# Kernel tuning notes

Hardware: AMD Instinct MI355X
Metric: run time of the kernel (lower is better)

## Reference

```python
import jax, jax.numpy as jnp
import numpy as np

E = 21   # numParticipants (experts)
D = 128  # input features (hardcoded Linear(128,16))
H = 16   # hidden
N = 262144  # rows


def setup_inputs() -> dict:
    key = jax.random.key(0)
    ks = jax.random.split(key, 6)
    x = jax.random.normal(ks[0], (N, D), dtype=jnp.float32)
    sid = jax.random.randint(ks[1], (N,), 0, E)
    s1 = 1.0 / np.sqrt(D)
    W1 = jax.random.uniform(ks[2], (E, D, H), jnp.float32, -s1, s1)
    b1 = jax.random.uniform(ks[3], (E, H), jnp.float32, -s1, s1)
    s2 = 1.0 / np.sqrt(H)
    W2 = jax.random.uniform(ks[4], (E, H), jnp.float32, -s2, s2)  # Linear(16,1) weight, squeezed
    b2 = jax.random.uniform(ks[5], (E,), jnp.float32, -s2, s2)
    return {"x": x, "sid": sid, "W1": W1, "b1": b1, "W2": W2, "b2": b2}


def reference(x, sid, W1, b1, W2, b2):
    # Per-row expert MLP: h = relu(x @ W1[sid] + b1[sid]); y = relu(h . W2[sid] + b2[sid]).
    # Dropout(0.5) is identity in eval mode. Vectorized routing: compute first layer for
    # all 21 tiny experts ([N,E,H] ~ 350MB), then select the routed expert per row.
    h_all = jax.nn.relu(jnp.einsum('nd,edh->neh', x, W1) + b1[None, :, :])  # [N,E,H]
    h = jnp.take_along_axis(h_all, sid[:, None, None], axis=1)[:, 0, :]      # [N,H]
    y = jax.nn.relu(jnp.einsum('nh,nh->n', h, W2[sid]) + b2[sid])            # [N]
    return y[:, None]  # [N,1]
```

## Files before the change

kernel.cpp:

```cpp
#include <hip/hip_runtime.h>
#include <stdint.h>

#define N_ROWS 262144
#define DIM    128
#define HID    16
#define NEXP   21
#define NSEG   (N_ROWS / 64 + NEXP)
#define NBLK1  256
#define RPB    (N_ROWS / NBLK1)
#define RPT    (RPB / 256)

__global__ __launch_bounds__(256) void k_hist(const int* __restrict__ sid,
                                              int* __restrict__ counts,
                                              int* __restrict__ blockBase) {
    __shared__ int lh[NEXP];
    int t = threadIdx.x;
    if (t < NEXP) lh[t] = 0;
    __syncthreads();
    int base = blockIdx.x * RPB + t;
#pragma unroll
    for (int r = 0; r < RPT; r++) {
        atomicAdd(&lh[sid[base + r * 256]], 1);
    }
    __syncthreads();
    if (t < NEXP) blockBase[blockIdx.x * NEXP + t] = atomicAdd(&counts[t], lh[t]);
}

__global__ __launch_bounds__(256) void k_scatter(const int* __restrict__ sid,
                                                 const int* __restrict__ counts,
                                                 const int* __restrict__ blockBase,
                                                 int* __restrict__ buckets) {
    __shared__ int sbase[NEXP];
    __shared__ int lcur[NEXP];
    int t = threadIdx.x;
    if (t == 0) {
        int acc = 0;
        for (int e = 0; e < NEXP; e++) {
            sbase[e] = acc + blockBase[blockIdx.x * NEXP + e];
            acc += ((counts[e] + 63) >> 6) << 6;
        }
    }
    if (t < NEXP) lcur[t] = 0;
    __syncthreads();
    int base = blockIdx.x * RPB + t;
#pragma unroll
    for (int r = 0; r < RPT; r++) {
        int row = base + r * 256;
        int e = sid[row];
        int lp = atomicAdd(&lcur[e], 1);
        buckets[sbase[e] + lp] = row | (e << 24);
    }
}

typedef __attribute__((ext_vector_type(8))) short bf16x8;
typedef __attribute__((ext_vector_type(4))) float f32x4;

__device__ __forceinline__ uint32_t pack2(uint32_t a, uint32_t b) {
    return __builtin_amdgcn_perm(b, a, 0x07060302u);
}

__device__ __forceinline__ void cvt8(const float* f, bf16x8& fh, bf16x8& fl) {
    union { uint32_t u[4]; bf16x8 v; } H, L;
#pragma unroll
    for (int i = 0; i < 4; i++) {
        uint32_t a = __float_as_uint(f[2 * i]);
        uint32_t b = __float_as_uint(f[2 * i + 1]);
        H.u[i] = pack2(a, b);
        float ra = f[2 * i]     - __uint_as_float(a & 0xffff0000u);
        float rb = f[2 * i + 1] - __uint_as_float(b & 0xffff0000u);
        L.u[i] = pack2(__float_as_uint(ra), __float_as_uint(rb));
    }
    fh = H.v; fl = L.v;
}

__global__ __launch_bounds__(256, 4) void k_mfma(const float* __restrict__ x,
                                                 const float* __restrict__ W1,
                                                 const float* __restrict__ b1,
                                                 const float* __restrict__ W2,
                                                 const float* __restrict__ b2,
                                                 const int* __restrict__ buckets,
                                                 float* __restrict__ out) {
    const int seg = blockIdx.x * 4 + (threadIdx.x >> 6);
    if (seg >= NSEG) return;
    const int lane = threadIdx.x & 63;

    const int ent = buckets[seg * 64 + lane];
    if (__ballot(ent >= 0) == 0ULL) return;
    const int e = __builtin_amdgcn_readfirstlane(ent) >> 24;
    const int row0 = __shfl(ent, 0, 64) & 0x00FFFFFF;
    const int vrow = (ent >= 0) ? (ent & 0x00FFFFFF) : row0;

    const int ncol  = lane & 15;
    const int kbase = (lane >> 4) * 8;

    int arow[4];
#pragma unroll
    for (int mt = 0; mt < 4; mt++) arow[mt] = __shfl(vrow, mt * 16 + ncol, 64);

    const float* __restrict__ w1 = W1 + e * (DIM * HID);
    const float b1v = b1[e * HID + ncol];
    const float w2v = W2[e * HID + ncol];
    const float b2v = b2[e];

    const f32x4 zero = {0.0f, 0.0f, 0.0f, 0.0f};
    f32x4 acc[4] = {zero, zero, zero, zero};

#pragma unroll 1
    for (int kt = 0; kt < 4; kt++) {
        float bf[8];
        const float* wp = w1 + (kt * 32 + kbase) * HID + ncol;
#pragma unroll
        for (int t = 0; t < 8; t++) bf[t] = wp[t * HID];
        bf16x8 bh, bl;
        cvt8(bf, bh, bl);

#pragma unroll
        for (int mt = 0; mt < 4; mt++) {
            const float* xp = x + (size_t)arow[mt] * DIM + kt * 32 + kbase;
            float af[8];
            *(float4*)(af)     = *(const float4*)(xp);
            *(float4*)(af + 4) = *(const float4*)(xp + 4);
            bf16x8 ah, al;
            cvt8(af, ah, al);
            acc[mt] = __builtin_amdgcn_mfma_f32_16x16x32_bf16(ah, bh, acc[mt], 0, 0, 0);
            acc[mt] = __builtin_amdgcn_mfma_f32_16x16x32_bf16(al, bh, acc[mt], 0, 0, 0);
            acc[mt] = __builtin_amdgcn_mfma_f32_16x16x32_bf16(ah, bl, acc[mt], 0, 0, 0);
        }
    }

#pragma unroll
    for (int mt = 0; mt < 4; mt++) {
#pragma unroll
        for (int r = 0; r < 4; r++) {
            float c = fmaxf(acc[mt][r] + b1v, 0.0f) * w2v;
            c += __shfl_xor(c, 1, 64);
            c += __shfl_xor(c, 2, 64);
            c += __shfl_xor(c, 4, 64);
            c += __shfl_xor(c, 8, 64);
            const int slot = mt * 16 + (lane >> 4) * 4 + r;
            const int sent = __shfl(ent, slot, 64);
            if (ncol == 0 && sent >= 0)
                out[sent & 0x00FFFFFF] = fmaxf(c + b2v, 0.0f);
        }
    }
}

__global__ __launch_bounds__(256) void k_naive(const float* __restrict__ x,
                                               const int* __restrict__ sid,
                                               const float* __restrict__ W1,
                                               const float* __restrict__ b1,
                                               const float* __restrict__ W2,
                                               const float* __restrict__ b2,
                                               float* __restrict__ out) {
    int row = blockIdx.x * 256 + threadIdx.x;
    if (row >= N_ROWS) return;
    int e = sid[row];
    const float* w1 = W1 + e * (DIM * HID);
    const float* xr = x + (size_t)row * DIM;
    float h[HID];
#pragma unroll
    for (int j = 0; j < HID; j++) h[j] = b1[e * HID + j];
    for (int k = 0; k < DIM; k++) {
        float xk = xr[k];
#pragma unroll
        for (int j = 0; j < HID; j++) h[j] = fmaf(xk, w1[k * HID + j], h[j]);
    }
    float acc = b2[e];
#pragma unroll
    for (int j = 0; j < HID; j++) acc = fmaf(fmaxf(h[j], 0.0f), W2[e * HID + j], acc);
    out[row] = fmaxf(acc, 0.0f);
}

extern "C" void kernel_launch(void* const* d_in, const int* in_sizes, int n_in,
                              void* d_out, int out_size, void* d_ws, size_t ws_size,
                              hipStream_t stream) {
    const float* x   = (const float*)d_in[0];
    const int*   sid = (const int*)d_in[1];
    const float* W1  = (const float*)d_in[2];
    const float* b1  = (const float*)d_in[3];
    const float* W2  = (const float*)d_in[4];
    const float* b2  = (const float*)d_in[5];
    float* out = (float*)d_out;

    const size_t bucketBytes = (size_t)NSEG * 64 * sizeof(int);
    const size_t countBytes  = 32 * sizeof(int);
    const size_t bbBytes     = (size_t)NBLK1 * NEXP * sizeof(int);
    const size_t need = bucketBytes + countBytes + bbBytes;

    if (ws_size < need) {
        k_naive<<<(N_ROWS + 255) / 256, 256, 0, stream>>>(x, sid, W1, b1, W2, b2, out);
        return;
    }

    char* ws = (char*)d_ws;
    int* buckets   = (int*)ws;
    int* counts    = (int*)(ws + bucketBytes);
    int* blockBase = (int*)(ws + bucketBytes + countBytes);

    hipMemsetAsync(buckets, 0xFF, bucketBytes, stream);
    hipMemsetAsync(counts, 0, countBytes, stream);
    k_hist<<<NBLK1, 256, 0, stream>>>(sid, counts, blockBase);
    k_scatter<<<NBLK1, 256, 0, stream>>>(sid, counts, blockBase, buckets);
    k_mfma<<<(NSEG + 3) / 4, 256, 0, stream>>>(x, W1, b1, W2, b2, buckets, out);
}
```

Baseline: 220.9 us.

## Fuse histogram and scatter into one cooperative routing kernel with grid sync

Replaces two memsets plus the separate histogram and scatter kernels with a single cooperative kernel. Each block counts its rows, then a grid-wide sync lets every block compute its own prefix offsets from all blocks' counts, and the block scatters its rows into padded expert buckets. Block 0 writes the -1 padding instead of a full-buffer memset. This removes several launches and the memset traffic, but adds a grid barrier and a redundant 256x21 prefix scan in every block. If the cooperative launch fails, it falls back to the old path.

```diff
diff --git a/kernel.cpp b/kernel.cpp
--- a/kernel.cpp
+++ b/kernel.cpp
@@ -1,5 +1,8 @@
 #include <hip/hip_runtime.h>
+#include <hip/hip_cooperative_groups.h>
 #include <stdint.h>
+
+namespace cg = cooperative_groups;
 
 #define N_ROWS 262144
 #define DIM    128
@@ -9,6 +12,78 @@
 #define NBLK1  256
 #define RPB    (N_ROWS / NBLK1)
 #define RPT    (RPB / 256)
+
+__global__ __launch_bounds__(256) void k_route(const int* __restrict__ sid,
+                                               int* __restrict__ blockCnt,
+                                               int* __restrict__ buckets) {
+    __shared__ int lh[NEXP];
+    __shared__ int wbase[NEXP];
+    __shared__ int lcur[NEXP];
+    __shared__ int ebase[NEXP + 1];
+    __shared__ int cnt_s[NBLK1 * NEXP];
+
+    const int t = threadIdx.x;
+    const int b = blockIdx.x;
+    if (t < NEXP) lh[t] = 0;
+    __syncthreads();
+
+    int er[RPT];
+    const int rbase = b * RPB + t;
+#pragma unroll
+    for (int r = 0; r < RPT; r++) {
+        er[r] = sid[rbase + r * 256];
+        atomicAdd(&lh[er[r]], 1);
+    }
+    __syncthreads();
+    if (t < NEXP) blockCnt[b * NEXP + t] = lh[t];
+
+    __threadfence();
+    cg::this_grid().sync();
+
+    for (int i = t; i < NBLK1 * NEXP; i += 256) cnt_s[i] = blockCnt[i];
+    __syncthreads();
+
+    if (t < NEXP) {
+        int pre = 0, tot = 0;
+#pragma unroll 8
+        for (int bb = 0; bb < NBLK1; bb++) {
+            int v = cnt_s[bb * NEXP + t];
+            pre += (bb < b) ? v : 0;
+            tot += v;
+        }
+        lh[t] = tot;
+        wbase[t] = pre;
+        lcur[t] = 0;
+    }
+    __syncthreads();
+    if (t == 0) {
+        int acc = 0;
+        for (int e = 0; e < NEXP; e++) {
+            ebase[e] = acc;
+            acc += ((lh[e] + 63) >> 6) << 6;
+        }
+        ebase[NEXP] = acc;
+    }
+    __syncthreads();
+    if (t < NEXP) wbase[t] += ebase[t];
+    __syncthreads();
+
+#pragma unroll
+    for (int r = 0; r < RPT; r++) {
+        const int e = er[r];
+        const int lp = atomicAdd(&lcur[e], 1);
+        buckets[wbase[e] + lp] = (rbase + r * 256) | (e << 24);
+    }
+
+    if (b == 0) {
+        for (int e = 0; e < NEXP; e++) {
+            const int s = ebase[e] + lh[e];
+            const int eend = ebase[e + 1];
+            for (int i = s + t; i < eend; i += 256) buckets[i] = -1;
+        }
+        for (int i = ebase[NEXP] + t; i < NSEG * 64; i += 256) buckets[i] = -1;
+    }
+}
 
 __global__ __launch_bounds__(256) void k_hist(const int* __restrict__ sid,
                                               int* __restrict__ counts,
@@ -183,9 +258,9 @@
     float* out = (float*)d_out;
 
     const size_t bucketBytes = (size_t)NSEG * 64 * sizeof(int);
+    const size_t bcBytes     = (size_t)NBLK1 * NEXP * sizeof(int);
     const size_t countBytes  = 32 * sizeof(int);
-    const size_t bbBytes     = (size_t)NBLK1 * NEXP * sizeof(int);
-    const size_t need = bucketBytes + countBytes + bbBytes;
+    const size_t need = bucketBytes + bcBytes + countBytes;
 
     if (ws_size < need) {
         k_naive<<<(N_ROWS + 255) / 256, 256, 0, stream>>>(x, sid, W1, b1, W2, b2, out);
@@ -193,13 +268,23 @@
     }
 
     char* ws = (char*)d_ws;
-    int* buckets   = (int*)ws;
-    int* counts    = (int*)(ws + bucketBytes);
-    int* blockBase = (int*)(ws + bucketBytes + countBytes);
-
-    hipMemsetAsync(buckets, 0xFF, bucketBytes, stream);
-    hipMemsetAsync(counts, 0, countBytes, stream);
-    k_hist<<<NBLK1, 256, 0, stream>>>(sid, counts, blockBase);
-    k_scatter<<<NBLK1, 256, 0, stream>>>(sid, counts, blockBase, buckets);
+    int* buckets  = (int*)ws;
+    int* blockCnt = (int*)(ws + bucketBytes);
+    int* counts   = (int*)(ws + bucketBytes + bcBytes);
+
+    const int* sid_ = sid;
+    int* bc_ = blockCnt;
+    int* bk_ = buckets;
+    void* args[] = {(void*)&sid_, (void*)&bc_, (void*)&bk_};
+    hipError_t cerr = hipLaunchCooperativeKernel((const void*)k_route,
+                                                 dim3(NBLK1), dim3(256),
+                                                 args, 0, stream);
+    if (cerr != hipSuccess) {
+        hipMemsetAsync(buckets, 0xFF, bucketBytes, stream);
+        hipMemsetAsync(counts, 0, countBytes, stream);
+        k_hist<<<NBLK1, 256, 0, stream>>>(sid, counts, blockCnt);
+        k_scatter<<<NBLK1, 256, 0, stream>>>(sid, counts, blockCnt, buckets);
+    }
+
     k_mfma<<<(NSEG + 3) / 4, 256, 0, stream>>>(x, W1, b1, W2, b2, buckets, out);
 }
```

New measurement: 267.9 us. 21.3% more time.

## Fuse histogram and scatter into one routing kernel with fixed per-expert regions

Applied to the files above, without the earlier changes.

Merges the histogram and scatter kernels into a single routing kernel. It keeps each thread's sid values in registers and writes rows into fixed-capacity per-expert bucket regions, so no global prefix is needed. The MFMA kernel now finds each segment's expert and valid-row count from the counts array instead of reading sentinel-filled buckets, which removes the bucket memset and one kernel launch. In exchange, every wave reads all 21 counts in a small loop, and the bucket workspace grows to a fixed capacity per expert that would overflow if one expert received more than 262144 rows.

```diff
diff --git a/kernel.cpp b/kernel.cpp
--- a/kernel.cpp
+++ b/kernel.cpp
@@ -10,45 +10,37 @@
 #define RPB    (N_ROWS / NBLK1)
 #define RPT    (RPB / 256)
 
-__global__ __launch_bounds__(256) void k_hist(const int* __restrict__ sid,
-                                              int* __restrict__ counts,
-                                              int* __restrict__ blockBase) {
+#define CAPSEG 4096
+#define REGION (CAPSEG * 64)
+
+__global__ __launch_bounds__(256) void k_route(const int* __restrict__ sid,
+                                               int* __restrict__ counts,
+                                               int* __restrict__ buckets) {
     __shared__ int lh[NEXP];
-    int t = threadIdx.x;
+    __shared__ int sbase[NEXP];
+    __shared__ int lcur[NEXP];
+    const int t = threadIdx.x;
     if (t < NEXP) lh[t] = 0;
     __syncthreads();
-    int base = blockIdx.x * RPB + t;
+
+    int er[RPT];
+    const int rbase = blockIdx.x * RPB + t;
 #pragma unroll
     for (int r = 0; r < RPT; r++) {
-        atomicAdd(&lh[sid[base + r * 256]], 1);
+        er[r] = sid[rbase + r * 256];
+        atomicAdd(&lh[er[r]], 1);
     }
     __syncthreads();
-    if (t < NEXP) blockBase[blockIdx.x * NEXP + t] = atomicAdd(&counts[t], lh[t]);
-}
-
-__global__ __launch_bounds__(256) void k_scatter(const int* __restrict__ sid,
-                                                 const int* __restrict__ counts,
-                                                 const int* __restrict__ blockBase,
-                                                 int* __restrict__ buckets) {
-    __shared__ int sbase[NEXP];
-    __shared__ int lcur[NEXP];
-    int t = threadIdx.x;
-    if (t == 0) {
-        int acc = 0;
-        for (int e = 0; e < NEXP; e++) {
-            sbase[e] = acc + blockBase[blockIdx.x * NEXP + e];
-            acc += ((counts[e] + 63) >> 6) << 6;
-        }
-    }
-    if (t < NEXP) lcur[t] = 0;
+    if (t < NEXP) {
+        sbase[t] = atomicAdd(&counts[t], lh[t]);
+        lcur[t] = 0;
+    }
     __syncthreads();
-    int base = blockIdx.x * RPB + t;
 #pragma unroll
     for (int r = 0; r < RPT; r++) {
-        int row = base + r * 256;
-        int e = sid[row];
-        int lp = atomicAdd(&lcur[e], 1);
-        buckets[sbase[e] + lp] = row | (e << 24);
+        const int e = er[r];
+        const int lp = atomicAdd(&lcur[e], 1);
+        buckets[e * REGION + sbase[e] + lp] = rbase + r * 256;
     }
 }
 
@@ -78,17 +70,30 @@
                                                  const float* __restrict__ b1,
                                                  const float* __restrict__ W2,
                                                  const float* __restrict__ b2,
+                                                 const int* __restrict__ counts,
                                                  const int* __restrict__ buckets,
                                                  float* __restrict__ out) {
     const int seg = blockIdx.x * 4 + (threadIdx.x >> 6);
-    if (seg >= NSEG) return;
+
+    int e = -1, ls = 0, rem = 0, cum = 0;
+#pragma unroll
+    for (int i = 0; i < NEXP; i++) {
+        const int c = counts[i];
+        const int ns = (c + 63) >> 6;
+        if (e < 0 && seg < cum + ns) {
+            e = i;
+            ls = seg - cum;
+            const int left = c - ls * 64;
+            rem = left < 64 ? left : 64;
+        }
+        cum += ns;
+    }
+    if (e < 0) return;
+
     const int lane = threadIdx.x & 63;
-
-    const int ent = buckets[seg * 64 + lane];
-    if (__ballot(ent >= 0) == 0ULL) return;
-    const int e = __builtin_amdgcn_readfirstlane(ent) >> 24;
-    const int row0 = __shfl(ent, 0, 64) & 0x00FFFFFF;
-    const int vrow = (ent >= 0) ? (ent & 0x00FFFFFF) : row0;
+    const int ent = buckets[e * REGION + ls * 64 + lane];
+    const int row0 = __shfl(ent, 0, 64);
+    const int vrow = (lane < rem) ? ent : row0;
 
     const int ncol  = lane & 15;
     const int kbase = (lane >> 4) * 8;
@@ -138,9 +143,9 @@
             c += __shfl_xor(c, 4, 64);
             c += __shfl_xor(c, 8, 64);
             const int slot = mt * 16 + (lane >> 4) * 4 + r;
-            const int sent = __shfl(ent, slot, 64);
-            if (ncol == 0 && sent >= 0)
-                out[sent & 0x00FFFFFF] = fmaxf(c + b2v, 0.0f);
+            const int srow = __shfl(vrow, slot, 64);
+            if (ncol == 0 && slot < rem)
+                out[srow] = fmaxf(c + b2v, 0.0f);
         }
     }
 }
@@ -182,10 +187,9 @@
     const float* b2  = (const float*)d_in[5];
     float* out = (float*)d_out;
 
-    const size_t bucketBytes = (size_t)NSEG * 64 * sizeof(int);
+    const size_t bucketBytes = (size_t)NEXP * REGION * sizeof(int);
     const size_t countBytes  = 32 * sizeof(int);
-    const size_t bbBytes     = (size_t)NBLK1 * NEXP * sizeof(int);
-    const size_t need = bucketBytes + countBytes + bbBytes;
+    const size_t need = bucketBytes + countBytes;
 
     if (ws_size < need) {
         k_naive<<<(N_ROWS + 255) / 256, 256, 0, stream>>>(x, sid, W1, b1, W2, b2, out);
@@ -193,13 +197,10 @@
     }
 
     char* ws = (char*)d_ws;
-    int* buckets   = (int*)ws;
-    int* counts    = (int*)(ws + bucketBytes);
-    int* blockBase = (int*)(ws + bucketBytes + countBytes);
-
-    hipMemsetAsync(buckets, 0xFF, bucketBytes, stream);
+    int* buckets = (int*)ws;
+    int* counts  = (int*)(ws + bucketBytes);
+
     hipMemsetAsync(counts, 0, countBytes, stream);
-    k_hist<<<NBLK1, 256, 0, stream>>>(sid, counts, blockBase);
-    k_scatter<<<NBLK1, 256, 0, stream>>>(sid, counts, blockBase, buckets);
-    k_mfma<<<(NSEG + 3) / 4, 256, 0, stream>>>(x, W1, b1, W2, b2, buckets, out);
-}
+    k_route<<<NBLK1, 256, 0, stream>>>(sid, counts, buckets);
+    k_mfma<<<(NSEG + 3) / 4, 256, 0, stream>>>(x, W1, b1, W2, b2, counts, buckets, out);
+}
```

Result: faster. 216.2 us (-2.1%).
